# Performance work log

Hardware: AMD Instinct MI355X
Metric: run time of the kernel (lower is better)

The kernel has to match this reference:

```python
import jax, jax.numpy as jnp
import numpy as np

BETA = 0.25


def setup_inputs() -> dict:
    key = jax.random.key(0)
    k1, k2, k3 = jax.random.split(key, 3)
    B, T, D, K = 4, 2048, 512, 16384
    z_e = jax.random.normal(k1, (B, T, D), dtype=jnp.float32)
    codebook = jax.random.normal(k2, (K, D), dtype=jnp.float32)  # frozen embedding
    # nn.Linear(D, D, bias=False) weight, scaled like kaiming-uniform magnitude
    W = jax.random.normal(k3, (D, D), dtype=jnp.float32) * (1.0 / np.sqrt(D))
    return {"z_e": z_e, "codebook": codebook, "W": W}


def reference(z_e, codebook, W):
    B, T, D = z_e.shape
    # effective codebook: Linear(codebook) = codebook @ W.T   -> (K, D)
    eff = jnp.matmul(codebook, W.T)
    z_flat = z_e.reshape(-1, D)  # (N, D)
    # squared euclidean distances (argmin-equivalent to cdist p=2)
    d2 = (
        jnp.sum(z_flat * z_flat, axis=1, keepdims=True)  # (N,1)
        - 2.0 * jnp.matmul(z_flat, eff.T)                  # (N,K)
        + jnp.sum(eff * eff, axis=1)[None, :]              # (1,K)
    )
    code_indices = jnp.argmin(d2, axis=1)  # (N,)
    z_q = eff[code_indices].reshape(B, T, D)
    loss_w = jnp.mean((jax.lax.stop_gradient(z_e) - z_q) ** 2)
    loss_commit = BETA * jnp.mean((z_e - jax.lax.stop_gradient(z_q)) ** 2)
    total_loss = loss_w + loss_commit
    # straight-through estimator
    z_q_out = z_e + jax.lax.stop_gradient(z_q - z_e)
    return z_q_out, total_loss, code_indices.reshape(B, T)
```

## Files before the change

### kernel.cpp

```cpp
#include <hip/hip_runtime.h>
#include <stdint.h>


#define N_ROWS 8192
#define DIM    512
#define K_CB   16384
#define TILE_F16 16384
#define HALF_F16 8192
#define KT_EFF 24
#define KT_D   8
#define PAN_D   ((size_t)KT_D * TILE_F16)
#define RMARGIN 4.0f

typedef _Float16 f16x8 __attribute__((ext_vector_type(8)));
typedef float f32x4 __attribute__((ext_vector_type(4)));

#define FENCE() asm volatile("" ::: "memory")
#define BARRIER() do { FENCE(); __builtin_amdgcn_s_barrier(); FENCE(); } while (0)
#define VMCNT(n) asm volatile("s_waitcnt vmcnt(" #n ")" ::: "memory")

__device__ __forceinline__ void gload_lds16(const void* g, void* l) {
  __builtin_amdgcn_global_load_lds(
      (const __attribute__((address_space(1))) uint32_t*)g,
      (__attribute__((address_space(3))) uint32_t*)l, 16, 0, 0);
}


__device__ __forceinline__ void stage_half(const _Float16* src, _Float16* ldsb,
                                           int w, int lane) {
  const _Float16* s = src + w * 512 + lane * 8;
  _Float16* l = ldsb + w * 512;
  gload_lds16(s, l);
  gload_lds16(s + 4096, l + 4096);
}

template <int MQ>
__device__ __forceinline__ void read_a(const _Float16* At, int wr, int lh, int lq,
                                       f16x8 af[4][2]) {
#pragma unroll
  for (int m2 = 0; m2 < 4; ++m2) {
    const int row = wr * 128 + (MQ * 4 + m2) * 16 + lh;
    const int half = row >> 7, r = row & 127;
#pragma unroll
    for (int kk = 0; kk < 2; ++kk) {
      const int kblk = kk * 4 + lq;
      af[m2][kk] = *reinterpret_cast<const f16x8*>(
          &At[(((size_t)(half * 8 + kblk)) * 128 + r) * 8]);
    }
  }
}

template <int NQ>
__device__ __forceinline__ void read_b(const _Float16* Bt, int wc, int lh, int lq,
                                       f16x8 bf[4][2]) {
#pragma unroll
  for (int n2 = 0; n2 < 2; ++n2) {
    const int row = wc * 64 + (NQ * 2 + n2) * 16 + lh;
    const int half = row >> 7, r = row & 127;
#pragma unroll
    for (int kk = 0; kk < 2; ++kk) {
      const int kblk = kk * 4 + lq;
      bf[NQ * 2 + n2][kk] = *reinterpret_cast<const f16x8*>(
          &Bt[(((size_t)(half * 8 + kblk)) * 128 + r) * 8]);
    }
  }
}

template <int MQ, int NQ>
__device__ __forceinline__ void mfma_phase(const f16x8 af[4][2],
                                           const f16x8 bf[4][2],
                                           f32x4 acc[8][4]) {
  __builtin_amdgcn_s_setprio(1);
#pragma unroll
  for (int kk = 0; kk < 2; ++kk)
#pragma unroll
    for (int m2 = 0; m2 < 4; ++m2)
#pragma unroll
      for (int n2 = 0; n2 < 2; ++n2)
        acc[MQ * 4 + m2][NQ * 2 + n2] = __builtin_amdgcn_mfma_f32_16x16x32_f16(
            af[m2][kk], bf[NQ * 2 + n2][kk], acc[MQ * 4 + m2][NQ * 2 + n2], 0, 0, 0);
  __builtin_amdgcn_s_setprio(0);
}

__device__ __forceinline__ void pipeline8(
    const _Float16* Abase, const _Float16* Bbase,
    _Float16 (&lds)[4][TILE_F16], f32x4 (&acc)[8][4],
    int w, int lane, int wr, int wc, int lh, int lq, int NT) {
  f16x8 af[4][2], bf[4][2];
  stage_half(Abase, &lds[0][0], w, lane);
  stage_half(Abase + HALF_F16, &lds[0][HALF_F16], w, lane);
  stage_half(Bbase, &lds[1][0], w, lane);
  stage_half(Bbase + HALF_F16, &lds[1][HALF_F16], w, lane);
  stage_half(Bbase + TILE_F16, &lds[3][0], w, lane);
  stage_half(Bbase + TILE_F16 + HALF_F16, &lds[3][HALF_F16], w, lane);
  stage_half(Abase + TILE_F16, &lds[2][0], w, lane);
  VMCNT(6);
  BARRIER();
  for (int t = 0; t < NT; ++t) {
    const int s = t & 1;
    const _Float16* At = &lds[s * 2 + 0][0];
    const _Float16* Bt = &lds[s * 2 + 1][0];
    read_a<0>(At, wr, lh, lq, af);
    read_b<0>(Bt, wc, lh, lq, bf);
    if (t + 1 < NT)
      stage_half(Abase + (size_t)(t + 1) * TILE_F16 + HALF_F16,
                 &lds[(s ^ 1) * 2][HALF_F16], w, lane);
    BARRIER();
    mfma_phase<0, 0>(af, bf, acc);
    BARRIER();
    read_b<1>(Bt, wc, lh, lq, bf);
    BARRIER();
    mfma_phase<0, 1>(af, bf, acc);
    BARRIER();
    read_a<1>(At, wr, lh, lq, af);
    if (t + 2 < NT)
      stage_half(Bbase + (size_t)(t + 2) * TILE_F16, &lds[s * 2 + 1][0], w, lane);
    BARRIER();
    mfma_phase<1, 1>(af, bf, acc);
    BARRIER();
    if (t + 2 < NT) {
      stage_half(Bbase + (size_t)(t + 2) * TILE_F16 + HALF_F16,
                 &lds[s * 2 + 1][HALF_F16], w, lane);
      stage_half(Abase + (size_t)(t + 2) * TILE_F16, &lds[s * 2][0], w, lane);
    }
    BARRIER();
    mfma_phase<1, 0>(af, bf, acc);
    if (t == NT - 2) { VMCNT(0); } else { VMCNT(6); }
    BARRIER();
  }
}

__global__ __launch_bounds__(256) void split_tiled_kernel(
    const float* __restrict__ S, _Float16* __restrict__ T, int resid_limb) {
  const int b = blockIdx.x;
  const int mp = b / 48;
  const int r1 = b % 48;
  const int kt = r1 >> 1, half = r1 & 1;
  const int limb = kt >> 3;
  const int ksrc = (kt & 7) * 64;
  const bool resid = (limb == resid_limb);
  const int t = threadIdx.x;
  _Float16* dst = T + ((size_t)(mp * KT_EFF + kt) * 2 + half) * HALF_F16;
#pragma unroll
  for (int cc = 0; cc < 4; ++cc) {
    const int ci = cc * 256 + t;
    const int kblk = ci >> 7, row = ci & 127;
    const int m = mp * 256 + half * 128 + row;
    const float* src = &S[(size_t)m * DIM + ksrc + kblk * 8];
    float4 x0 = *reinterpret_cast<const float4*>(src);
    float4 x1 = *reinterpret_cast<const float4*>(src + 4);
    const float xs[8] = {x0.x, x0.y, x0.z, x0.w, x1.x, x1.y, x1.z, x1.w};
    f16x8 o;
    if (!resid) {
#pragma unroll
      for (int j = 0; j < 8; ++j) o[j] = (_Float16)xs[j];
    } else {
#pragma unroll
      for (int j = 0; j < 8; ++j) {
        _Float16 h = (_Float16)xs[j];
        o[j] = (_Float16)(xs[j] - (float)h);
      }
    }
    *reinterpret_cast<f16x8*>(&dst[(size_t)ci * 8]) = o;
  }
}

__global__ __launch_bounds__(256) void split1_kernel(
    const float* __restrict__ S, _Float16* __restrict__ T) {
  const int b = blockIdx.x;
  const int p = b >> 4;
  const int r1 = b & 15;
  const int kt = r1 >> 1, half = r1 & 1;
  const int ksrc = kt * 64;
  const int t = threadIdx.x;
  _Float16* dst = T + ((size_t)(p * KT_D + kt) * 2 + half) * HALF_F16;
#pragma unroll
  for (int cc = 0; cc < 4; ++cc) {
    const int ci = cc * 256 + t;
    const int kblk = ci >> 7, row = ci & 127;
    const int m = p * 256 + half * 128 + row;
    const float* src = &S[(size_t)m * DIM + ksrc + kblk * 8];
    float4 x0 = *reinterpret_cast<const float4*>(src);
    float4 x1 = *reinterpret_cast<const float4*>(src + 4);
    const float xs[8] = {x0.x, x0.y, x0.z, x0.w, x1.x, x1.y, x1.z, x1.w};
    f16x8 o;
#pragma unroll
    for (int j = 0; j < 8; ++j) o[j] = (_Float16)xs[j];
    *reinterpret_cast<f16x8*>(&dst[(size_t)ci * 8]) = o;
  }
}

__global__ __launch_bounds__(256) void effgemm128_kernel(
    const _Float16* __restrict__ CpT, const _Float16* __restrict__ WpT,
    float* __restrict__ eff, _Float16* __restrict__ BpT) {
  __shared__ __align__(16) _Float16 lbuf[2][2][HALF_F16];
  const int tid = threadIdx.x;
  const int w = tid >> 6, lane = tid & 63;
  const int lh = lane & 15, lq = lane >> 4;
  const int wr = w >> 1, wc = w & 1;
  const int bid = blockIdx.x;
  const int nb = bid & 3, mh = bid >> 2;
  const int pA = mh >> 1, hA = mh & 1;
  const int pB = nb >> 1, hB = nb & 1;
  f32x4 acc[4][4] = {};

  auto stage = [&](int kt, int buf) {
    const _Float16* a = CpT + (((size_t)pA * KT_EFF + kt) * 2 + hA) * HALF_F16;
    const _Float16* b = WpT + (((size_t)pB * KT_EFF + kt) * 2 + hB) * HALF_F16;
#pragma unroll
    for (int i = 0; i < 4; ++i) {
      const int off = i * 2048 + w * 512;
      gload_lds16(a + off + lane * 8, &lbuf[buf][0][off]);
      gload_lds16(b + off + lane * 8, &lbuf[buf][1][off]);
    }
  };

  stage(0, 0);
  for (int kt = 0; kt < KT_EFF; ++kt) {
    __syncthreads();
    if (kt + 1 < KT_EFF) stage(kt + 1, (kt + 1) & 1);
    const _Float16* At = &lbuf[kt & 1][0][0];
    const _Float16* Bt = &lbuf[kt & 1][1][0];
    f16x8 af[4][2], bf[4][2];
#pragma unroll
    for (int mf = 0; mf < 4; ++mf) {
      const int r = wr * 64 + mf * 16 + lh;
#pragma unroll
      for (int kk = 0; kk < 2; ++kk)
        af[mf][kk] = *reinterpret_cast<const f16x8*>(
            &At[((kk * 4 + lq) * 128 + r) * 8]);
    }
#pragma unroll
    for (int nf = 0; nf < 4; ++nf) {
      const int r = wc * 64 + nf * 16 + lh;
#pragma unroll
      for (int kk = 0; kk < 2; ++kk)
        bf[nf][kk] = *reinterpret_cast<const f16x8*>(
            &Bt[((kk * 4 + lq) * 128 + r) * 8]);
    }
    __builtin_amdgcn_s_setprio(1);
#pragma unroll
    for (int kk = 0; kk < 2; ++kk)
#pragma unroll
      for (int mf = 0; mf < 4; ++mf)
#pragma unroll
        for (int nf = 0; nf < 4; ++nf)
          acc[mf][nf] = __builtin_amdgcn_mfma_f32_16x16x32_f16(
              af[mf][kk], bf[nf][kk], acc[mf][nf], 0, 0, 0);
    __builtin_amdgcn_s_setprio(0);
  }

#pragma unroll
  for (int mf = 0; mf < 4; ++mf)
#pragma unroll
    for (int nf = 0; nf < 4; ++nf)
#pragma unroll
      for (int j = 0; j < 4; ++j) {
        const int rl = wr * 64 + mf * 16 + lq * 4 + j;
        const int cl = wc * 64 + nf * 16 + lh;
        const int row = mh * 128 + rl;
        const int col = nb * 128 + cl;
        const float v = acc[mf][nf][j];
        eff[(size_t)row * DIM + col] = v;
        const int ktd = col >> 6, kblk = (col >> 3) & 7, ce = col & 7;
        BpT[((((size_t)(row >> 8) * KT_D + ktd) * 2 + ((row >> 7) & 1)) * 8 + kblk)
                * 1024 + (row & 127) * 8 + ce] = (_Float16)v;
      }
}

__global__ __launch_bounds__(256) void effnorm_kernel(
    const float* __restrict__ E, float* __restrict__ En) {
  const int w = threadIdx.x >> 6;
  const int lane = threadIdx.x & 63;
  const int row = blockIdx.x * 4 + w;
  const float* er = &E[(size_t)row * DIM];
  float s = 0.f;
#pragma unroll
  for (int k = 0; k < DIM / 64; ++k) {
    float v = er[lane + k * 64];
    s = fmaf(v, v, s);
  }
#pragma unroll
  for (int o = 32; o; o >>= 1) s += __shfl_down(s, o, 64);
  if (lane == 0) En[row] = s;
}

__global__ __launch_bounds__(512) void dist1_kernel(
    const _Float16* __restrict__ ApT, const _Float16* __restrict__ BpT,
    const float* __restrict__ En, float* __restrict__ gv,
    unsigned* __restrict__ gmask) {
  __shared__ __align__(16) _Float16 lds[4][TILE_F16];
  const int tid = threadIdx.x;
  const int w = tid >> 6, lane = tid & 63;
  const int lh = lane & 15, lq = lane >> 4;
  const int wr = w >> 2, wc = w & 3;
  const int bid = blockIdx.x;
  const int xcd = bid & 7, c = bid >> 3;
  const int np = xcd * 8 + (c & 7);
  const int mp = c >> 3;
  f32x4 acc[8][4] = {};
  pipeline8(ApT + (size_t)mp * PAN_D, BpT + (size_t)np * PAN_D, lds, acc,
            w, lane, wr, wc, lh, lq, KT_D);
  float en[4];
#pragma unroll
  for (int nf = 0; nf < 4; ++nf)
    en[nf] = En[np * 256 + wc * 64 + nf * 16 + lh];
#pragma unroll
  for (int mf = 0; mf < 8; ++mf) {
#pragma unroll
    for (int j = 0; j < 4; ++j) {
      const float s0 = fmaf(-2.f, acc[mf][0][j], en[0]);
      const float s1 = fmaf(-2.f, acc[mf][1][j], en[1]);
      const float s2 = fmaf(-2.f, acc[mf][2][j], en[2]);
      const float s3 = fmaf(-2.f, acc[mf][3][j], en[3]);
      float v0 = fminf(s0, s1);
      float v1 = fminf(s2, s3);
#pragma unroll
      for (int m = 1; m < 16; m <<= 1) {
        v0 = fminf(v0, __shfl_xor(v0, m, 64));
        v1 = fminf(v1, __shfl_xor(v1, m, 64));
      }
      const unsigned long long b0 = __ballot(s0 <= v0 + RMARGIN);
      const unsigned long long b1 = __ballot(s1 <= v0 + RMARGIN);
      const unsigned long long b2 = __ballot(s2 <= v1 + RMARGIN);
      const unsigned long long b3 = __ballot(s3 <= v1 + RMARGIN);
      if (lh == 0) {
        const int row = mp * 256 + wr * 128 + mf * 16 + lq * 4 + j;
        const unsigned w0 = (unsigned)((b0 >> (lq * 16)) & 0xFFFFull) |
                            ((unsigned)((b1 >> (lq * 16)) & 0xFFFFull) << 16);
        const unsigned w1 = (unsigned)((b2 >> (lq * 16)) & 0xFFFFull) |
                            ((unsigned)((b3 >> (lq * 16)) & 0xFFFFull) << 16);
        float2* gp = (float2*)&gv[(size_t)row * 512 + np * 8 + wc * 2];
        *gp = make_float2(v0, v1);
        uint2* mq = (uint2*)&gmask[(size_t)row * 512 + np * 8 + wc * 2];
        *mq = make_uint2(w0, w1);
      }
    }
  }
}

__global__ __launch_bounds__(256) void refine_kernel(
    const float* __restrict__ Z, const float* __restrict__ E,
    const float* __restrict__ En, const float* __restrict__ gv,
    const unsigned* __restrict__ gmask, float* __restrict__ zq,
    float* __restrict__ out_idx, float* __restrict__ ploss) {
  const int row = blockIdx.x * 4 + (threadIdx.x >> 6);
  const int lane = threadIdx.x & 63;
  const int hl = lane & 31;
  const int hi = lane >> 5;

  float v[8];
#pragma unroll
  for (int i = 0; i < 8; ++i) v[i] = gv[(size_t)row * 512 + i * 64 + lane];
  float A = fminf(fminf(fminf(v[0], v[1]), fminf(v[2], v[3])),
                  fminf(fminf(v[4], v[5]), fminf(v[6], v[7])));
#pragma unroll
  for (int m = 1; m < 64; m <<= 1) A = fminf(A, __shfl_xor(A, m, 64));
  const float thr = A + RMARGIN;

  float4 zr0, zr1, zr2, zr3;
  {
    const float4* zp = (const float4*)(Z + (size_t)row * 512 + hl * 16);
    zr0 = zp[0]; zr1 = zp[1]; zr2 = zp[2]; zr3 = zp[3];
  }

  float bv = 3.0e38f;
  int bi = 2147483647;
#pragma unroll 1
  for (int i = 0; i < 8; ++i) {
    unsigned long long bm = __ballot(v[i] <= thr);
    while (bm) {
      const int l = __builtin_ctzll(bm);
      bm &= bm - 1;
      const int g = i * 64 + l;
      unsigned m = gmask[(size_t)row * 512 + g];
      while (m) {
        const int c0 = __builtin_ctz(m);
        m &= m - 1;
        int c1 = -1;
        if (m) { c1 = __builtin_ctz(m); m &= m - 1; }
        const int cl = hi ? c1 : c0;
        const bool act = (cl >= 0);
        const int col = g * 32 + (act ? cl : c0);
        const float4* er = (const float4*)(E + (size_t)col * 512 + hl * 16);
        const float4 e0 = er[0], e1 = er[1], e2 = er[2], e3 = er[3];
        float p = 0.f;
        p = fmaf(zr0.x, e0.x, p); p = fmaf(zr0.y, e0.y, p);
        p = fmaf(zr0.z, e0.z, p); p = fmaf(zr0.w, e0.w, p);
        p = fmaf(zr1.x, e1.x, p); p = fmaf(zr1.y, e1.y, p);
        p = fmaf(zr1.z, e1.z, p); p = fmaf(zr1.w, e1.w, p);
        p = fmaf(zr2.x, e2.x, p); p = fmaf(zr2.y, e2.y, p);
        p = fmaf(zr2.z, e2.z, p); p = fmaf(zr2.w, e2.w, p);
        p = fmaf(zr3.x, e3.x, p); p = fmaf(zr3.y, e3.y, p);
        p = fmaf(zr3.z, e3.z, p); p = fmaf(zr3.w, e3.w, p);
#pragma unroll
        for (int s2 = 1; s2 < 32; s2 <<= 1) p += __shfl_xor(p, s2, 64);
        const float vv = fmaf(-2.f, p, En[col]);
        if (act && (vv < bv || (vv == bv && col < bi))) { bv = vv; bi = col; }
      }
    }
  }
#pragma unroll
  for (int s2 = 1; s2 < 64; s2 <<= 1) {
    const float v2 = __shfl_xor(bv, s2, 64);
    const int i2 = __shfl_xor(bi, s2, 64);
    if (v2 < bv || (v2 == bv && i2 < bi)) { bv = v2; bi = i2; }
  }
  const int idx = bi;

  const float4* e4 = (const float4*)(E + (size_t)idx * 512 + lane * 8);
  const float4* z4 = (const float4*)(Z + (size_t)row * 512 + lane * 8);
  float4* q4 = (float4*)(zq + (size_t)row * 512 + lane * 8);
  const float4 ea = e4[0], eb = e4[1];
  const float4 za = z4[0], zb = z4[1];
  q4[0] = ea; q4[1] = eb;
  float s = 0.f;
  s = fmaf(za.x - ea.x, za.x - ea.x, s); s = fmaf(za.y - ea.y, za.y - ea.y, s);
  s = fmaf(za.z - ea.z, za.z - ea.z, s); s = fmaf(za.w - ea.w, za.w - ea.w, s);
  s = fmaf(zb.x - eb.x, zb.x - eb.x, s); s = fmaf(zb.y - eb.y, zb.y - eb.y, s);
  s = fmaf(zb.z - eb.z, zb.z - eb.z, s); s = fmaf(zb.w - eb.w, zb.w - eb.w, s);
#pragma unroll
  for (int o = 32; o; o >>= 1) s += __shfl_down(s, o, 64);
  if (lane == 0) {
    ploss[row] = s;
    out_idx[row] = (float)idx;
  }
}

__global__ __launch_bounds__(256) void loss_final_kernel(
    const float* __restrict__ ploss, float* __restrict__ out_loss) {
  const int t = threadIdx.x;
  double s = 0.0;
  for (int i = t; i < N_ROWS; i += 256) s += (double)ploss[i];
#pragma unroll
  for (int o = 32; o; o >>= 1) s += __shfl_down(s, o, 64);
  __shared__ double ds[4];
  if ((t & 63) == 0) ds[t >> 6] = s;
  __syncthreads();
  if (t == 0) {
    double tot = ds[0] + ds[1] + ds[2] + ds[3];
    out_loss[0] = (float)(1.25 * tot / ((double)N_ROWS * (double)DIM));
  }
}


extern "C" void kernel_launch(void* const* d_in, const int* in_sizes, int n_in,
                              void* d_out, int out_size, void* d_ws, size_t ws_size,
                              hipStream_t stream) {
  const float* z_e      = (const float*)d_in[0];
  const float* codebook = (const float*)d_in[1];
  const float* W        = (const float*)d_in[2];
  float* out = (float*)d_out;
  char* ws = (char*)d_ws;

  float*          eff     = (float*)(ws);
  float*          effnorm = (float*)(ws + 33554432);
  _Float16*       WpT     = (_Float16*)(ws + 33619968);
  float*          ploss   = (float*)(ws + 36274176);
  _Float16*       CpT     = (_Float16*)(ws + 36306944);
  float*          gv      = (float*)(ws + 36306944);
  _Float16*       ApT     = (_Float16*)(ws + 53084160);
  unsigned*       gmask   = (unsigned*)(ws + 61472768);
  _Float16*       BpT     = (_Float16*)(ws + 86638592);

  float* out_zq   = out;
  float* out_loss = out + (size_t)N_ROWS * DIM;
  float* out_idx  = out + (size_t)N_ROWS * DIM + 1;

  split_tiled_kernel<<<64 * 48, 256, 0, stream>>>(codebook, CpT, 2);
  split_tiled_kernel<<<2 * 48, 256, 0, stream>>>(W, WpT, 1);
  effgemm128_kernel<<<512, 256, 0, stream>>>(CpT, WpT, eff, BpT);
  effnorm_kernel<<<K_CB / 4, 256, 0, stream>>>(eff, effnorm);
  split1_kernel<<<32 * 16, 256, 0, stream>>>(z_e, ApT);
  dist1_kernel<<<2048, 512, 0, stream>>>(ApT, BpT, effnorm, gv, gmask);
  refine_kernel<<<N_ROWS / 4, 256, 0, stream>>>(z_e, eff, effnorm, gv, gmask,
                                                out_zq, out_idx, ploss);
  loss_final_kernel<<<1, 256, 0, stream>>>(ploss, out_loss);
}
```

Before: 282.0 us.

## Switch distance GEMM screening pass from fp16 to fp8 MFMA

Converts the z_e rows and the effective codebook to fp8 in a repacked tile layout and runs the coarse distance GEMM with fp8 MFMA instructions, halving operand bytes through global memory and LDS. The refine pass margin grows to absorb the larger fp8 rounding error. In exchange, more candidates may survive the screening and need exact rechecking in the refine kernel. If the margin is not wide enough, the chosen argmin could be wrong.

Measured after the change: 295.6 us. +4.8%, slower.

```diff
diff --git a/kernel.cpp b/kernel.cpp
--- a/kernel.cpp
+++ b/kernel.cpp
@@ -9,11 +9,14 @@
 #define HALF_F16 8192
 #define KT_EFF 24
 #define KT_D   8
-#define PAN_D   ((size_t)KT_D * TILE_F16)
-#define RMARGIN 4.0f
+#define TILE_P8 16384
+#define HALF_P8 8192
+#define PAN_P8  ((size_t)KT_D * TILE_P8)
+#define RMARGIN 28.0f
 
 typedef _Float16 f16x8 __attribute__((ext_vector_type(8)));
 typedef float f32x4 __attribute__((ext_vector_type(4)));
+typedef long lx2 __attribute__((ext_vector_type(2)));
 
 #define FENCE() asm volatile("" ::: "memory")
 #define BARRIER() do { FENCE(); __builtin_amdgcn_s_barrier(); FENCE(); } while (0)
@@ -25,109 +28,10 @@
       (__attribute__((address_space(3))) uint32_t*)l, 16, 0, 0);
 }
 
-
-__device__ __forceinline__ void stage_half(const _Float16* src, _Float16* ldsb,
-                                           int w, int lane) {
-  const _Float16* s = src + w * 512 + lane * 8;
-  _Float16* l = ldsb + w * 512;
-  gload_lds16(s, l);
-  gload_lds16(s + 4096, l + 4096);
-}
-
-template <int MQ>
-__device__ __forceinline__ void read_a(const _Float16* At, int wr, int lh, int lq,
-                                       f16x8 af[4][2]) {
-#pragma unroll
-  for (int m2 = 0; m2 < 4; ++m2) {
-    const int row = wr * 128 + (MQ * 4 + m2) * 16 + lh;
-    const int half = row >> 7, r = row & 127;
-#pragma unroll
-    for (int kk = 0; kk < 2; ++kk) {
-      const int kblk = kk * 4 + lq;
-      af[m2][kk] = *reinterpret_cast<const f16x8*>(
-          &At[(((size_t)(half * 8 + kblk)) * 128 + r) * 8]);
-    }
-  }
-}
-
-template <int NQ>
-__device__ __forceinline__ void read_b(const _Float16* Bt, int wc, int lh, int lq,
-                                       f16x8 bf[4][2]) {
-#pragma unroll
-  for (int n2 = 0; n2 < 2; ++n2) {
-    const int row = wc * 64 + (NQ * 2 + n2) * 16 + lh;
-    const int half = row >> 7, r = row & 127;
-#pragma unroll
-    for (int kk = 0; kk < 2; ++kk) {
-      const int kblk = kk * 4 + lq;
-      bf[NQ * 2 + n2][kk] = *reinterpret_cast<const f16x8*>(
-          &Bt[(((size_t)(half * 8 + kblk)) * 128 + r) * 8]);
-    }
-  }
-}
-
-template <int MQ, int NQ>
-__device__ __forceinline__ void mfma_phase(const f16x8 af[4][2],
-                                           const f16x8 bf[4][2],
-                                           f32x4 acc[8][4]) {
-  __builtin_amdgcn_s_setprio(1);
-#pragma unroll
-  for (int kk = 0; kk < 2; ++kk)
-#pragma unroll
-    for (int m2 = 0; m2 < 4; ++m2)
-#pragma unroll
-      for (int n2 = 0; n2 < 2; ++n2)
-        acc[MQ * 4 + m2][NQ * 2 + n2] = __builtin_amdgcn_mfma_f32_16x16x32_f16(
-            af[m2][kk], bf[NQ * 2 + n2][kk], acc[MQ * 4 + m2][NQ * 2 + n2], 0, 0, 0);
-  __builtin_amdgcn_s_setprio(0);
-}
-
-__device__ __forceinline__ void pipeline8(
-    const _Float16* Abase, const _Float16* Bbase,
-    _Float16 (&lds)[4][TILE_F16], f32x4 (&acc)[8][4],
-    int w, int lane, int wr, int wc, int lh, int lq, int NT) {
-  f16x8 af[4][2], bf[4][2];
-  stage_half(Abase, &lds[0][0], w, lane);
-  stage_half(Abase + HALF_F16, &lds[0][HALF_F16], w, lane);
-  stage_half(Bbase, &lds[1][0], w, lane);
-  stage_half(Bbase + HALF_F16, &lds[1][HALF_F16], w, lane);
-  stage_half(Bbase + TILE_F16, &lds[3][0], w, lane);
-  stage_half(Bbase + TILE_F16 + HALF_F16, &lds[3][HALF_F16], w, lane);
-  stage_half(Abase + TILE_F16, &lds[2][0], w, lane);
-  VMCNT(6);
-  BARRIER();
-  for (int t = 0; t < NT; ++t) {
-    const int s = t & 1;
-    const _Float16* At = &lds[s * 2 + 0][0];
-    const _Float16* Bt = &lds[s * 2 + 1][0];
-    read_a<0>(At, wr, lh, lq, af);
-    read_b<0>(Bt, wc, lh, lq, bf);
-    if (t + 1 < NT)
-      stage_half(Abase + (size_t)(t + 1) * TILE_F16 + HALF_F16,
-                 &lds[(s ^ 1) * 2][HALF_F16], w, lane);
-    BARRIER();
-    mfma_phase<0, 0>(af, bf, acc);
-    BARRIER();
-    read_b<1>(Bt, wc, lh, lq, bf);
-    BARRIER();
-    mfma_phase<0, 1>(af, bf, acc);
-    BARRIER();
-    read_a<1>(At, wr, lh, lq, af);
-    if (t + 2 < NT)
-      stage_half(Bbase + (size_t)(t + 2) * TILE_F16, &lds[s * 2 + 1][0], w, lane);
-    BARRIER();
-    mfma_phase<1, 1>(af, bf, acc);
-    BARRIER();
-    if (t + 2 < NT) {
-      stage_half(Bbase + (size_t)(t + 2) * TILE_F16 + HALF_F16,
-                 &lds[s * 2 + 1][HALF_F16], w, lane);
-      stage_half(Abase + (size_t)(t + 2) * TILE_F16, &lds[s * 2][0], w, lane);
-    }
-    BARRIER();
-    mfma_phase<1, 0>(af, bf, acc);
-    if (t == NT - 2) { VMCNT(0); } else { VMCNT(6); }
-    BARRIER();
-  }
+__device__ __forceinline__ unsigned cvt2_fp8(float a, float b) {
+  unsigned r;
+  asm("v_cvt_pk_fp8_f32 %0, %1, %2" : "=v"(r) : "v"(a), "v"(b));
+  return r & 0xFFFFu;
 }
 
 __global__ __launch_bounds__(256) void split_tiled_kernel(
@@ -166,14 +70,14 @@
 }
 
 __global__ __launch_bounds__(256) void split1_kernel(
-    const float* __restrict__ S, _Float16* __restrict__ T) {
+    const float* __restrict__ S, uint8_t* __restrict__ T) {
   const int b = blockIdx.x;
   const int p = b >> 4;
   const int r1 = b & 15;
   const int kt = r1 >> 1, half = r1 & 1;
   const int ksrc = kt * 64;
   const int t = threadIdx.x;
-  _Float16* dst = T + ((size_t)(p * KT_D + kt) * 2 + half) * HALF_F16;
+  uint8_t* dst = T + ((size_t)(p * KT_D + kt) * 2 + half) * HALF_P8;
 #pragma unroll
   for (int cc = 0; cc < 4; ++cc) {
     const int ci = cc * 256 + t;
@@ -182,17 +86,18 @@
     const float* src = &S[(size_t)m * DIM + ksrc + kblk * 8];
     float4 x0 = *reinterpret_cast<const float4*>(src);
     float4 x1 = *reinterpret_cast<const float4*>(src + 4);
-    const float xs[8] = {x0.x, x0.y, x0.z, x0.w, x1.x, x1.y, x1.z, x1.w};
-    f16x8 o;
-#pragma unroll
-    for (int j = 0; j < 8; ++j) o[j] = (_Float16)xs[j];
-    *reinterpret_cast<f16x8*>(&dst[(size_t)ci * 8]) = o;
+    const unsigned lo = cvt2_fp8(x0.x, x0.y) | (cvt2_fp8(x0.z, x0.w) << 16);
+    const unsigned hi = cvt2_fp8(x1.x, x1.y) | (cvt2_fp8(x1.z, x1.w) << 16);
+    const uint64_t pack = (uint64_t)lo | ((uint64_t)hi << 32);
+    const int q = kblk & 3, h2 = kblk >> 2;
+    *reinterpret_cast<uint64_t*>(&dst[(size_t)(q * 128 + row) * 16 + h2 * 8]) =
+        pack;
   }
 }
 
 __global__ __launch_bounds__(256) void effgemm128_kernel(
     const _Float16* __restrict__ CpT, const _Float16* __restrict__ WpT,
-    float* __restrict__ eff, _Float16* __restrict__ BpT) {
+    float* __restrict__ eff, uint8_t* __restrict__ BpT) {
   __shared__ __align__(16) _Float16 lbuf[2][2][HALF_F16];
   const int tid = threadIdx.x;
   const int w = tid >> 6, lane = tid & 63;
@@ -253,19 +158,24 @@
 #pragma unroll
   for (int mf = 0; mf < 4; ++mf)
 #pragma unroll
-    for (int nf = 0; nf < 4; ++nf)
+    for (int nf = 0; nf < 4; ++nf) {
+      const int cl = wc * 64 + nf * 16 + lh;
+      const int col = nb * 128 + cl;
+      const int ktd = col >> 6, kd = col & 63;
+      const int q = (kd >> 3) & 3, h2 = kd >> 5, jb = kd & 7;
+      const unsigned c01 = cvt2_fp8(acc[mf][nf][0], acc[mf][nf][1]);
+      const unsigned c23 = cvt2_fp8(acc[mf][nf][2], acc[mf][nf][3]);
 #pragma unroll
       for (int j = 0; j < 4; ++j) {
         const int rl = wr * 64 + mf * 16 + lq * 4 + j;
-        const int cl = wc * 64 + nf * 16 + lh;
         const int row = mh * 128 + rl;
-        const int col = nb * 128 + cl;
-        const float v = acc[mf][nf][j];
-        eff[(size_t)row * DIM + col] = v;
-        const int ktd = col >> 6, kblk = (col >> 3) & 7, ce = col & 7;
-        BpT[((((size_t)(row >> 8) * KT_D + ktd) * 2 + ((row >> 7) & 1)) * 8 + kblk)
-                * 1024 + (row & 127) * 8 + ce] = (_Float16)v;
+        eff[(size_t)row * DIM + col] = acc[mf][nf][j];
+        const unsigned byte =
+            (j < 2 ? (c01 >> (j * 8)) : (c23 >> ((j - 2) * 8))) & 255u;
+        BpT[((((size_t)(row >> 8) * KT_D + ktd) * 2 + ((row >> 7) & 1)) * 4 + q)
+                * 2048 + (row & 127) * 16 + h2 * 8 + jb] = (uint8_t)byte;
       }
+    }
 }
 
 __global__ __launch_bounds__(256) void effnorm_kernel(
@@ -285,11 +195,103 @@
   if (lane == 0) En[row] = s;
 }
 
+
+__device__ __forceinline__ void stage_half8(const uint8_t* src, uint8_t* ldsb,
+                                            int tid) {
+  gload_lds16(src + tid * 16, ldsb + tid * 16);
+}
+
+template <int MQ>
+__device__ __forceinline__ void read_a8(const uint8_t* At, int wr, int lh, int lq,
+                                        lx2 af[4]) {
+#pragma unroll
+  for (int m2 = 0; m2 < 4; ++m2) {
+    const int row = wr * 128 + (MQ * 4 + m2) * 16 + lh;
+    const int half = row >> 7, r = row & 127;
+    af[m2] = *reinterpret_cast<const lx2*>(
+        &At[(size_t)half * 8192 + (lq * 128 + r) * 16]);
+  }
+}
+
+template <int NQ>
+__device__ __forceinline__ void read_b8(const uint8_t* Bt, int wc, int lh, int lq,
+                                        lx2 bf[4]) {
+#pragma unroll
+  for (int n2 = 0; n2 < 2; ++n2) {
+    const int row = wc * 64 + (NQ * 2 + n2) * 16 + lh;
+    const int half = row >> 7, r = row & 127;
+    bf[NQ * 2 + n2] = *reinterpret_cast<const lx2*>(
+        &Bt[(size_t)half * 8192 + (lq * 128 + r) * 16]);
+  }
+}
+
+template <int MQ, int NQ>
+__device__ __forceinline__ void mfma_phase8(const lx2 af[4], const lx2 bf[4],
+                                            f32x4 acc[8][4]) {
+  __builtin_amdgcn_s_setprio(1);
+#pragma unroll
+  for (int kk = 0; kk < 2; ++kk)
+#pragma unroll
+    for (int m2 = 0; m2 < 4; ++m2)
+#pragma unroll
+      for (int n2 = 0; n2 < 2; ++n2)
+        acc[MQ * 4 + m2][NQ * 2 + n2] = __builtin_amdgcn_mfma_f32_16x16x32_fp8_fp8(
+            af[m2][kk], bf[NQ * 2 + n2][kk], acc[MQ * 4 + m2][NQ * 2 + n2], 0, 0, 0);
+  __builtin_amdgcn_s_setprio(0);
+}
+
+__device__ __forceinline__ void pipeline8_p8(
+    const uint8_t* Ab, const uint8_t* Bb, uint8_t (&lds)[4][TILE_P8],
+    f32x4 (&acc)[8][4], int tid, int wr, int wc, int lh, int lq, int NT) {
+  lx2 af[4], bf[4];
+  stage_half8(Ab, &lds[0][0], tid);
+  stage_half8(Ab + HALF_P8, &lds[0][HALF_P8], tid);
+  stage_half8(Bb, &lds[1][0], tid);
+  stage_half8(Bb + HALF_P8, &lds[1][HALF_P8], tid);
+  stage_half8(Bb + TILE_P8, &lds[3][0], tid);
+  stage_half8(Bb + TILE_P8 + HALF_P8, &lds[3][HALF_P8], tid);
+  stage_half8(Ab + TILE_P8, &lds[2][0], tid);
+  VMCNT(3);
+  BARRIER();
+  for (int t = 0; t < NT; ++t) {
+    const int s = t & 1;
+    const uint8_t* At = &lds[s * 2 + 0][0];
+    const uint8_t* Bt = &lds[s * 2 + 1][0];
+    read_a8<0>(At, wr, lh, lq, af);
+    read_b8<0>(Bt, wc, lh, lq, bf);
+    if (t + 1 < NT)
+      stage_half8(Ab + (size_t)(t + 1) * TILE_P8 + HALF_P8,
+                  &lds[(s ^ 1) * 2][HALF_P8], tid);
+    BARRIER();
+    mfma_phase8<0, 0>(af, bf, acc);
+    BARRIER();
+    read_b8<1>(Bt, wc, lh, lq, bf);
+    BARRIER();
+    mfma_phase8<0, 1>(af, bf, acc);
+    BARRIER();
+    read_a8<1>(At, wr, lh, lq, af);
+    if (t + 2 < NT)
+      stage_half8(Bb + (size_t)(t + 2) * TILE_P8, &lds[s * 2 + 1][0], tid);
+    BARRIER();
+    mfma_phase8<1, 1>(af, bf, acc);
+    BARRIER();
+    if (t + 2 < NT) {
+      stage_half8(Bb + (size_t)(t + 2) * TILE_P8 + HALF_P8,
+                  &lds[s * 2 + 1][HALF_P8], tid);
+      stage_half8(Ab + (size_t)(t + 2) * TILE_P8, &lds[s * 2][0], tid);
+    }
+    BARRIER();
+    mfma_phase8<1, 0>(af, bf, acc);
+    if (t == NT - 2) { VMCNT(0); } else { VMCNT(3); }
+    BARRIER();
+  }
+}
+
 __global__ __launch_bounds__(512) void dist1_kernel(
-    const _Float16* __restrict__ ApT, const _Float16* __restrict__ BpT,
+    const uint8_t* __restrict__ ApT, const uint8_t* __restrict__ BpT,
     const float* __restrict__ En, float* __restrict__ gv,
     unsigned* __restrict__ gmask) {
-  __shared__ __align__(16) _Float16 lds[4][TILE_F16];
+  __shared__ __align__(16) uint8_t lds[4][TILE_P8];
   const int tid = threadIdx.x;
   const int w = tid >> 6, lane = tid & 63;
   const int lh = lane & 15, lq = lane >> 4;
@@ -299,8 +301,8 @@
   const int np = xcd * 8 + (c & 7);
   const int mp = c >> 3;
   f32x4 acc[8][4] = {};
-  pipeline8(ApT + (size_t)mp * PAN_D, BpT + (size_t)np * PAN_D, lds, acc,
-            w, lane, wr, wc, lh, lq, KT_D);
+  pipeline8_p8(ApT + (size_t)mp * PAN_P8, BpT + (size_t)np * PAN_P8, lds, acc,
+               tid, wr, wc, lh, lq, KT_D);
   float en[4];
 #pragma unroll
   for (int nf = 0; nf < 4; ++nf)
@@ -459,9 +461,9 @@
   float*          ploss   = (float*)(ws + 36274176);
   _Float16*       CpT     = (_Float16*)(ws + 36306944);
   float*          gv      = (float*)(ws + 36306944);
-  _Float16*       ApT     = (_Float16*)(ws + 53084160);
+  uint8_t*        ApT     = (uint8_t*)(ws + 53084160);
   unsigned*       gmask   = (unsigned*)(ws + 61472768);
-  _Float16*       BpT     = (_Float16*)(ws + 86638592);
+  uint8_t*        BpT     = (uint8_t*)(ws + 86638592);
 
   float* out_zq   = out;
   float* out_loss = out + (size_t)N_ROWS * DIM;
```

## Shrink distance GEMM tile to 128x128 for higher occupancy

Applied to the files above, without the earlier changes.

The distance kernel moves from 256x256 output tiles with four LDS tile buffers to 128x128 tiles with a smaller double-buffered LDS layout. Four times as many blocks are launched, and launch bounds request four blocks per CU so more waves can hide latency. Per-wave accumulators shrink, and each wave writes one min/mask pair per 32-column group instead of two, keeping the 512-entry gv/gmask layout. The cost is lower operand reuse, so global and LDS traffic per FLOP roughly doubles.

New measurement: 305.6 us. 8.4% more time.

```diff
diff --git a/kernel.cpp b/kernel.cpp
--- a/kernel.cpp
+++ b/kernel.cpp
@@ -9,7 +9,6 @@
 #define HALF_F16 8192
 #define KT_EFF 24
 #define KT_D   8
-#define PAN_D   ((size_t)KT_D * TILE_F16)
 #define RMARGIN 4.0f
 
 typedef _Float16 f16x8 __attribute__((ext_vector_type(8)));
@@ -24,7 +23,6 @@
       (const __attribute__((address_space(1))) uint32_t*)g,
       (__attribute__((address_space(3))) uint32_t*)l, 16, 0, 0);
 }
-
 
 __device__ __forceinline__ void stage_half(const _Float16* src, _Float16* ldsb,
                                            int w, int lane) {
@@ -32,102 +30,6 @@
   _Float16* l = ldsb + w * 512;
   gload_lds16(s, l);
   gload_lds16(s + 4096, l + 4096);
-}
-
-template <int MQ>
-__device__ __forceinline__ void read_a(const _Float16* At, int wr, int lh, int lq,
-                                       f16x8 af[4][2]) {
-#pragma unroll
-  for (int m2 = 0; m2 < 4; ++m2) {
-    const int row = wr * 128 + (MQ * 4 + m2) * 16 + lh;
-    const int half = row >> 7, r = row & 127;
-#pragma unroll
-    for (int kk = 0; kk < 2; ++kk) {
-      const int kblk = kk * 4 + lq;
-      af[m2][kk] = *reinterpret_cast<const f16x8*>(
-          &At[(((size_t)(half * 8 + kblk)) * 128 + r) * 8]);
-    }
-  }
-}
-
-template <int NQ>
-__device__ __forceinline__ void read_b(const _Float16* Bt, int wc, int lh, int lq,
-                                       f16x8 bf[4][2]) {
-#pragma unroll
-  for (int n2 = 0; n2 < 2; ++n2) {
-    const int row = wc * 64 + (NQ * 2 + n2) * 16 + lh;
-    const int half = row >> 7, r = row & 127;
-#pragma unroll
-    for (int kk = 0; kk < 2; ++kk) {
-      const int kblk = kk * 4 + lq;
-      bf[NQ * 2 + n2][kk] = *reinterpret_cast<const f16x8*>(
-          &Bt[(((size_t)(half * 8 + kblk)) * 128 + r) * 8]);
-    }
-  }
-}
-
-template <int MQ, int NQ>
-__device__ __forceinline__ void mfma_phase(const f16x8 af[4][2],
-                                           const f16x8 bf[4][2],
-                                           f32x4 acc[8][4]) {
-  __builtin_amdgcn_s_setprio(1);
-#pragma unroll
-  for (int kk = 0; kk < 2; ++kk)
-#pragma unroll
-    for (int m2 = 0; m2 < 4; ++m2)
-#pragma unroll
-      for (int n2 = 0; n2 < 2; ++n2)
-        acc[MQ * 4 + m2][NQ * 2 + n2] = __builtin_amdgcn_mfma_f32_16x16x32_f16(
-            af[m2][kk], bf[NQ * 2 + n2][kk], acc[MQ * 4 + m2][NQ * 2 + n2], 0, 0, 0);
-  __builtin_amdgcn_s_setprio(0);
-}
-
-__device__ __forceinline__ void pipeline8(
-    const _Float16* Abase, const _Float16* Bbase,
-    _Float16 (&lds)[4][TILE_F16], f32x4 (&acc)[8][4],
-    int w, int lane, int wr, int wc, int lh, int lq, int NT) {
-  f16x8 af[4][2], bf[4][2];
-  stage_half(Abase, &lds[0][0], w, lane);
-  stage_half(Abase + HALF_F16, &lds[0][HALF_F16], w, lane);
-  stage_half(Bbase, &lds[1][0], w, lane);
-  stage_half(Bbase + HALF_F16, &lds[1][HALF_F16], w, lane);
-  stage_half(Bbase + TILE_F16, &lds[3][0], w, lane);
-  stage_half(Bbase + TILE_F16 + HALF_F16, &lds[3][HALF_F16], w, lane);
-  stage_half(Abase + TILE_F16, &lds[2][0], w, lane);
-  VMCNT(6);
-  BARRIER();
-  for (int t = 0; t < NT; ++t) {
-    const int s = t & 1;
-    const _Float16* At = &lds[s * 2 + 0][0];
-    const _Float16* Bt = &lds[s * 2 + 1][0];
-    read_a<0>(At, wr, lh, lq, af);
-    read_b<0>(Bt, wc, lh, lq, bf);
-    if (t + 1 < NT)
-      stage_half(Abase + (size_t)(t + 1) * TILE_F16 + HALF_F16,
-                 &lds[(s ^ 1) * 2][HALF_F16], w, lane);
-    BARRIER();
-    mfma_phase<0, 0>(af, bf, acc);
-    BARRIER();
-    read_b<1>(Bt, wc, lh, lq, bf);
-    BARRIER();
-    mfma_phase<0, 1>(af, bf, acc);
-    BARRIER();
-    read_a<1>(At, wr, lh, lq, af);
-    if (t + 2 < NT)
-      stage_half(Bbase + (size_t)(t + 2) * TILE_F16, &lds[s * 2 + 1][0], w, lane);
-    BARRIER();
-    mfma_phase<1, 1>(af, bf, acc);
-    BARRIER();
-    if (t + 2 < NT) {
-      stage_half(Bbase + (size_t)(t + 2) * TILE_F16 + HALF_F16,
-                 &lds[s * 2 + 1][HALF_F16], w, lane);
-      stage_half(Abase + (size_t)(t + 2) * TILE_F16, &lds[s * 2][0], w, lane);
-    }
-    BARRIER();
-    mfma_phase<1, 0>(af, bf, acc);
-    if (t == NT - 2) { VMCNT(0); } else { VMCNT(6); }
-    BARRIER();
-  }
 }
 
 __global__ __launch_bounds__(256) void split_tiled_kernel(
@@ -285,55 +187,127 @@
   if (lane == 0) En[row] = s;
 }
 
-__global__ __launch_bounds__(512) void dist1_kernel(
+
+template <int MQ>
+__device__ __forceinline__ void d_read_a(const _Float16* At, int wr, int lh,
+                                         int lq, f16x8 af[4][2]) {
+#pragma unroll
+  for (int m2 = 0; m2 < 2; ++m2) {
+    const int r = wr * 64 + (MQ * 2 + m2) * 16 + lh;
+#pragma unroll
+    for (int kk = 0; kk < 2; ++kk)
+      af[MQ * 2 + m2][kk] = *reinterpret_cast<const f16x8*>(
+          &At[((kk * 4 + lq) * 128 + r) * 8]);
+  }
+}
+
+template <int NQ>
+__device__ __forceinline__ void d_read_b(const _Float16* Bt, int wc, int lh,
+                                         int lq, f16x8 bf[2][2]) {
+  const int r = wc * 32 + NQ * 16 + lh;
+#pragma unroll
+  for (int kk = 0; kk < 2; ++kk)
+    bf[NQ][kk] = *reinterpret_cast<const f16x8*>(
+        &Bt[((kk * 4 + lq) * 128 + r) * 8]);
+}
+
+template <int MQ, int NQ>
+__device__ __forceinline__ void d_mfma(const f16x8 af[4][2], const f16x8 bf[2][2],
+                                       f32x4 acc[4][2]) {
+  __builtin_amdgcn_s_setprio(1);
+#pragma unroll
+  for (int kk = 0; kk < 2; ++kk)
+#pragma unroll
+    for (int m2 = 0; m2 < 2; ++m2)
+      acc[MQ * 2 + m2][NQ] = __builtin_amdgcn_mfma_f32_16x16x32_f16(
+          af[MQ * 2 + m2][kk], bf[NQ][kk], acc[MQ * 2 + m2][NQ], 0, 0, 0);
+  __builtin_amdgcn_s_setprio(0);
+}
+
+__global__ __launch_bounds__(512, 4) void dist1_kernel(
     const _Float16* __restrict__ ApT, const _Float16* __restrict__ BpT,
     const float* __restrict__ En, float* __restrict__ gv,
     unsigned* __restrict__ gmask) {
-  __shared__ __align__(16) _Float16 lds[4][TILE_F16];
+  __shared__ __align__(16) _Float16 lds[2][2][HALF_F16];
   const int tid = threadIdx.x;
   const int w = tid >> 6, lane = tid & 63;
   const int lh = lane & 15, lq = lane >> 4;
   const int wr = w >> 2, wc = w & 3;
   const int bid = blockIdx.x;
   const int xcd = bid & 7, c = bid >> 3;
-  const int np = xcd * 8 + (c & 7);
-  const int mp = c >> 3;
-  f32x4 acc[8][4] = {};
-  pipeline8(ApT + (size_t)mp * PAN_D, BpT + (size_t)np * PAN_D, lds, acc,
-            w, lane, wr, wc, lh, lq, KT_D);
-  float en[4];
-#pragma unroll
-  for (int nf = 0; nf < 4; ++nf)
-    en[nf] = En[np * 256 + wc * 64 + nf * 16 + lh];
-#pragma unroll
-  for (int mf = 0; mf < 8; ++mf) {
+  const int nh = xcd * 16 + (c & 15);
+  const int mh = c >> 4;
+  const int pA = mh >> 1, hA = mh & 1;
+  const int pB = nh >> 1, hB = nh & 1;
+
+  auto Atile = [&](int kt) -> const _Float16* {
+    return ApT + (((size_t)pA * KT_D + kt) * 2 + hA) * HALF_F16;
+  };
+  auto Btile = [&](int kt) -> const _Float16* {
+    return BpT + (((size_t)pB * KT_D + kt) * 2 + hB) * HALF_F16;
+  };
+
+  float en[2];
+  en[0] = En[nh * 128 + wc * 32 + lh];
+  en[1] = En[nh * 128 + wc * 32 + 16 + lh];
+
+  f32x4 acc[4][2] = {};
+  f16x8 af[4][2], bf[2][2];
+
+  stage_half(Atile(0), &lds[0][0][0], w, lane);
+  stage_half(Btile(0), &lds[0][1][0], w, lane);
+  stage_half(Atile(1), &lds[1][0][0], w, lane);
+  stage_half(Btile(1), &lds[1][1][0], w, lane);
+  VMCNT(4);
+  BARRIER();
+
+  for (int t = 0; t < KT_D; ++t) {
+    const int s = t & 1;
+    const _Float16* At = &lds[s][0][0];
+    const _Float16* Bt = &lds[s][1][0];
+    d_read_a<0>(At, wr, lh, lq, af);
+    d_read_b<0>(Bt, wc, lh, lq, bf);
+    BARRIER();
+    d_mfma<0, 0>(af, bf, acc);
+    BARRIER();
+    d_read_b<1>(Bt, wc, lh, lq, bf);
+    BARRIER();
+    d_mfma<0, 1>(af, bf, acc);
+    BARRIER();
+    d_read_a<1>(At, wr, lh, lq, af);
+    BARRIER();
+    d_mfma<1, 1>(af, bf, acc);
+    BARRIER();
+    if (t + 2 < KT_D) {
+      stage_half(Atile(t + 2), &lds[s][0][0], w, lane);
+      stage_half(Btile(t + 2), &lds[s][1][0], w, lane);
+    }
+    BARRIER();
+    d_mfma<1, 0>(af, bf, acc);
+    if (t == KT_D - 2) { VMCNT(0); }
+    else if (t + 1 < KT_D) { VMCNT(4); }
+    BARRIER();
+  }
+
+  const int gidx = nh * 4 + wc;
+#pragma unroll
+  for (int mf = 0; mf < 4; ++mf) {
 #pragma unroll
     for (int j = 0; j < 4; ++j) {
       const float s0 = fmaf(-2.f, acc[mf][0][j], en[0]);
       const float s1 = fmaf(-2.f, acc[mf][1][j], en[1]);
-      const float s2 = fmaf(-2.f, acc[mf][2][j], en[2]);
-      const float s3 = fmaf(-2.f, acc[mf][3][j], en[3]);
       float v0 = fminf(s0, s1);
-      float v1 = fminf(s2, s3);
-#pragma unroll
-      for (int m = 1; m < 16; m <<= 1) {
+#pragma unroll
+      for (int m = 1; m < 16; m <<= 1)
         v0 = fminf(v0, __shfl_xor(v0, m, 64));
-        v1 = fminf(v1, __shfl_xor(v1, m, 64));
-      }
       const unsigned long long b0 = __ballot(s0 <= v0 + RMARGIN);
       const unsigned long long b1 = __ballot(s1 <= v0 + RMARGIN);
-      const unsigned long long b2 = __ballot(s2 <= v1 + RMARGIN);
-      const unsigned long long b3 = __ballot(s3 <= v1 + RMARGIN);
       if (lh == 0) {
-        const int row = mp * 256 + wr * 128 + mf * 16 + lq * 4 + j;
+        const int row = mh * 128 + wr * 64 + mf * 16 + lq * 4 + j;
         const unsigned w0 = (unsigned)((b0 >> (lq * 16)) & 0xFFFFull) |
                             ((unsigned)((b1 >> (lq * 16)) & 0xFFFFull) << 16);
-        const unsigned w1 = (unsigned)((b2 >> (lq * 16)) & 0xFFFFull) |
-                            ((unsigned)((b3 >> (lq * 16)) & 0xFFFFull) << 16);
-        float2* gp = (float2*)&gv[(size_t)row * 512 + np * 8 + wc * 2];
-        *gp = make_float2(v0, v1);
-        uint2* mq = (uint2*)&gmask[(size_t)row * 512 + np * 8 + wc * 2];
-        *mq = make_uint2(w0, w1);
+        gv[(size_t)row * 512 + gidx] = v0;
+        gmask[(size_t)row * 512 + gidx] = w0;
       }
     }
   }
@@ -472,7 +446,7 @@
   effgemm128_kernel<<<512, 256, 0, stream>>>(CpT, WpT, eff, BpT);
   effnorm_kernel<<<K_CB / 4, 256, 0, stream>>>(eff, effnorm);
   split1_kernel<<<32 * 16, 256, 0, stream>>>(z_e, ApT);
-  dist1_kernel<<<2048, 512, 0, stream>>>(ApT, BpT, effnorm, gv, gmask);
+  dist1_kernel<<<8192, 512, 0, stream>>>(ApT, BpT, effnorm, gv, gmask);
   refine_kernel<<<N_ROWS / 4, 256, 0, stream>>>(z_e, eff, effnorm, gv, gmask,
                                                 out_zq, out_idx, ploss);
   loss_final_kernel<<<1, 256, 0, stream>>>(ploss, out_loss);
```
